# Performance work log

Measured on AMD Instinct MI355X. Metric: run time of the kernel, lower is better.

## Reference

```python
import jax, jax.numpy as jnp
import numpy as np

# --- instant-NGP style multiresolution hash encoding config ---
L = 16          # levels
T = 524288      # hash table size (2**19)
D = 3           # input (spatial) dim
F = 2           # features per level
N_PTS = 500000  # query points
RES_MIN, RES_MAX = 16.0, 512.0

# spatial-hash primes from the source (first D entries; 1 for dim 0)
PRIMES = jnp.array([1, 2654435761, 805459861, 3674653429, 2097192037, 1434869437, 2165219737][:D], dtype=jnp.uint32)

# geometric resolution schedule N_l = floor(RES_MIN * b**l)
_b = np.exp((np.log(RES_MAX) - np.log(RES_MIN)) / (L - 1))
RES = jnp.asarray(np.floor(RES_MIN * _b ** np.arange(L)), dtype=jnp.float32)  # [L]

# the 2**D hypercube corner offsets, corner c has bit d = (c>>d)&1
OFFSETS = jnp.array([[(c >> d) & 1 for d in range(D)] for c in range(2 ** D)], dtype=jnp.uint32)  # [8, D]


def setup_inputs() -> dict:
    k1, k2 = jax.random.split(jax.random.key(0))
    x = jax.random.uniform(k1, (N_PTS, D), dtype=jnp.float32)          # coords in [0,1)
    hash_tables = jax.random.normal(k2, (L, T, F), dtype=jnp.float32) * 1e-4
    return {"x": x, "hash_tables": hash_tables}


def reference(x, hash_tables):
    N = x.shape[0]
    scaled = x[:, None, :] * RES[None, :, None]          # [N, L, D]
    floor = jnp.floor(scaled)
    w = scaled - floor                                    # [N, L, D] interpolation weights
    floor_u = floor.astype(jnp.uint32)

    # spatial hash of the 2**D corners: XOR-reduce(coord_d * prime_d) mod T.
    # loop over the D (=3) coordinate dims to avoid a [N,L,8,D] corner tensor.
    h = jnp.zeros((N, L, 2 ** D), dtype=jnp.uint32)
    for d in range(D):
        corner_d = floor_u[:, :, None, d] + OFFSETS[None, None, :, d]  # [N, L, 8], uint32 wrap
        h = h ^ (corner_d * PRIMES[d])
    idx = (h % jnp.uint32(T)).astype(jnp.int32)           # [N, L, 8]

    # gather per-level features: hash_tables[l, idx[n,l,c]] -> [N, L, 8, F]
    feats = hash_tables[jnp.arange(L)[None, :, None], idx]

    # D-linear interpolation weights: prod_d (w_d if corner bit set else 1-w_d)
    wd = jnp.where(OFFSETS[None, None, :, :] == 1, w[:, :, None, :], 1.0 - w[:, :, None, :])  # [N,L,8,D]
    weights = wd.prod(axis=-1)                            # [N, L, 8]

    out = (feats * weights[..., None]).sum(axis=2)        # [N, L, F]
    return out.reshape(N, L * F)
```

## Files before the change

### kernel.cpp

```cpp
#include <hip/hip_runtime.h>
#include <math.h>

#define NPTS 500000
#define TSIZE 524288u
#define TMASK (TSIZE - 1u)
#define CHUNKS 1954

struct ResArgs { float r[16]; };

__device__ __forceinline__ float2 mhe_point_level(
    const float* __restrict__ x, const float* __restrict__ tbl,
    int p, int l, float res)
{
    float x0 = x[p * 3 + 0];
    float x1 = x[p * 3 + 1];
    float x2 = x[p * 3 + 2];

    float s0 = x0 * res, s1 = x1 * res, s2 = x2 * res;
    float f0 = floorf(s0), f1 = floorf(s1), f2 = floorf(s2);
    float w0 = s0 - f0, w1 = s1 - f1, w2 = s2 - f2;
    unsigned u0 = (unsigned)f0, u1 = (unsigned)f1, u2 = (unsigned)f2;

    unsigned a0 = u0,               a1 = u0 + 1u;
    unsigned b0 = u1 * 2654435761u, b1 = (u1 + 1u) * 2654435761u;
    unsigned c0 = u2 * 805459861u,  c1 = (u2 + 1u) * 805459861u;

    const float2* t = (const float2*)tbl + (size_t)l * TSIZE;

    float v0a = 1.f - w0, v0b = w0;
    float v1a = 1.f - w1, v1b = w1;
    float v2a = 1.f - w2, v2b = w2;

    float o0 = 0.f, o1 = 0.f;
#pragma unroll
    for (int c = 0; c < 8; ++c) {
        unsigned h = ((c & 1) ? a1 : a0) ^ ((c & 2) ? b1 : b0) ^ ((c & 4) ? c1 : c0);
        float2 f = t[h & TMASK];
        float wgt = ((c & 1) ? v0b : v0a) * ((c & 2) ? v1b : v1a) * ((c & 4) ? v2b : v2a);
        o0 = fmaf(wgt, f.x, o0);
        o1 = fmaf(wgt, f.y, o1);
    }
    return make_float2(o0, o1);
}

__global__ __launch_bounds__(256) void mhe_gather(
    const float* __restrict__ x,
    const float* __restrict__ tbl,
    float2* __restrict__ ws,
    ResArgs ra)
{
    int b = blockIdx.x;
    int xcd = b & 7;
    int i = b >> 3;
    int l = xcd + ((i & 1) << 3);
    int p = (i >> 1) * 256 + threadIdx.x;
    if (p >= NPTS) return;

    float2 o = mhe_point_level(x, tbl, p, l, ra.r[l]);
    ws[(size_t)l * NPTS + p] = o;
}

__global__ __launch_bounds__(256) void mhe_transpose(
    const float2* __restrict__ ws, float2* __restrict__ out)
{
    __shared__ float2 tile[16][65];
    int p0 = blockIdx.x * 64;
    int t = threadIdx.x;

    int pc = t & 63;
#pragma unroll
    for (int i = 0; i < 4; ++i) {
        int l = (t >> 6) + i * 4;
        int p = p0 + pc;
        if (p < NPTS) tile[l][pc] = ws[(size_t)l * NPTS + p];
    }
    __syncthreads();

#pragma unroll
    for (int i = 0; i < 4; ++i) {
        int pp = (t >> 4) + i * 16;
        int l = t & 15;
        int p = p0 + pp;
        if (p < NPTS) out[(size_t)p * 16 + l] = tile[l][pp];
    }
}

__global__ __launch_bounds__(256) void mhe_kernel(
    const float* __restrict__ x,
    const float* __restrict__ tbl,
    float* __restrict__ out,
    ResArgs ra)
{
    int gid = blockIdx.x * 256 + threadIdx.x;
    int p = gid >> 4;
    int l = gid & 15;
    if (p >= NPTS) return;
    float2 o = mhe_point_level(x, tbl, p, l, ra.r[l]);
    ((float2*)out)[(size_t)p * 16 + l] = o;
}

extern "C" void kernel_launch(void* const* d_in, const int* in_sizes, int n_in,
                              void* d_out, int out_size, void* d_ws, size_t ws_size,
                              hipStream_t stream) {
    const float* x   = (const float*)d_in[0];
    const float* tbl = (const float*)d_in[1];
    float* out = (float*)d_out;

    ResArgs ra;
    double bb = exp((log(512.0) - log(16.0)) / 15.0);
    for (int l = 0; l < 16; ++l)
        ra.r[l] = (float)floor(16.0 * pow(bb, (double)l));

    size_t ws_needed = (size_t)NPTS * 16 * sizeof(float2);
    if (ws_size >= ws_needed) {
        mhe_gather<<<8 * 2 * CHUNKS, 256, 0, stream>>>(x, tbl, (float2*)d_ws, ra);
        mhe_transpose<<<(NPTS + 63) / 64, 256, 0, stream>>>((const float2*)d_ws,
                                                            (float2*)out);
    } else {
        mhe_kernel<<<(NPTS * 16 + 255) / 256, 256, 0, stream>>>(x, tbl, out, ra);
    }
}
```

Baseline: 241.4 us.

## Pair x-adjacent hash corners into float4 loads and reorder block-to-level mapping

When the x floor coordinate is even, the two x-corners hash to adjacent table entries (e and e^1), so one 16-byte float4 load fetches both and halves the gathers for those points. Odd x-coordinates issue a second float2 load for the other corner, which adds a divergent branch. Block scheduling now runs all chunks of levels 0-7 before levels 8-15, instead of interleaving them, to change cache locality across the per-level tables.

New measurement: 228.9 us. 1.05x faster.

```diff
diff --git a/kernel.cpp b/kernel.cpp
--- a/kernel.cpp
+++ b/kernel.cpp
@@ -21,24 +21,38 @@
     float w0 = s0 - f0, w1 = s1 - f1, w2 = s2 - f2;
     unsigned u0 = (unsigned)f0, u1 = (unsigned)f1, u2 = (unsigned)f2;
 
-    unsigned a0 = u0,               a1 = u0 + 1u;
     unsigned b0 = u1 * 2654435761u, b1 = (u1 + 1u) * 2654435761u;
     unsigned c0 = u2 * 805459861u,  c1 = (u2 + 1u) * 805459861u;
 
-    const float2* t = (const float2*)tbl + (size_t)l * TSIZE;
+    const float2* t  = (const float2*)tbl + (size_t)l * TSIZE;
+    const float4* t4 = (const float4*)t;
 
     float v0a = 1.f - w0, v0b = w0;
     float v1a = 1.f - w1, v1b = w1;
     float v2a = 1.f - w2, v2b = w2;
 
+    bool odd = (u0 & 1u) != 0u;
+    unsigned u0p1 = u0 + 1u;
+
     float o0 = 0.f, o1 = 0.f;
 #pragma unroll
-    for (int c = 0; c < 8; ++c) {
-        unsigned h = ((c & 1) ? a1 : a0) ^ ((c & 2) ? b1 : b0) ^ ((c & 4) ? c1 : c0);
-        float2 f = t[h & TMASK];
-        float wgt = ((c & 1) ? v0b : v0a) * ((c & 2) ? v1b : v1a) * ((c & 4) ? v2b : v2a);
-        o0 = fmaf(wgt, f.x, o0);
-        o1 = fmaf(wgt, f.y, o1);
+    for (int j = 0; j < 4; ++j) {
+        unsigned bc = ((j & 1) ? b1 : b0) ^ ((j & 2) ? c1 : c0);
+        unsigned e0 = (u0 ^ bc) & TMASK;
+        float4 q = t4[e0 >> 1];
+        float2 lo = make_float2(q.x, q.y);
+        float2 hi = make_float2(q.z, q.w);
+        float2 fc0 = (e0 & 1u) ? hi : lo;
+        float2 fc1 = (e0 & 1u) ? lo : hi;
+        if (odd) {
+            unsigned e1 = (u0p1 ^ bc) & TMASK;
+            fc1 = t[e1];
+        }
+        float wyz = ((j & 1) ? v1b : v1a) * ((j & 2) ? v2b : v2a);
+        o0 = fmaf(v0a * wyz, fc0.x, o0);
+        o1 = fmaf(v0a * wyz, fc0.y, o1);
+        o0 = fmaf(v0b * wyz, fc1.x, o0);
+        o1 = fmaf(v0b * wyz, fc1.y, o1);
     }
     return make_float2(o0, o1);
 }
@@ -52,8 +66,10 @@
     int b = blockIdx.x;
     int xcd = b & 7;
     int i = b >> 3;
-    int l = xcd + ((i & 1) << 3);
-    int p = (i >> 1) * 256 + threadIdx.x;
+    int half  = i >= CHUNKS;
+    int chunk = half ? i - CHUNKS : i;
+    int l = xcd + (half << 3);
+    int p = chunk * 256 + threadIdx.x;
     if (p >= NPTS) return;
 
     float2 o = mhe_point_level(x, tbl, p, l, ra.r[l]);
```
